# Kernel optimization log

Hardware: AMD Instinct MI355X
Metric: run time of the kernel (lower is better)

The kernel has to match this reference:

```python
import jax, jax.numpy as jnp
import numpy as np

LATENT = 64
HID = 64
IN_DIM = HID + 1  # 65
SLOPE = 0.2
EPS = 1e-8


def setup_inputs() -> dict:
    key = jax.random.key(0)
    ks = jax.random.split(key, 9)
    x = jax.random.normal(ks[0], (8192, LATENT, IN_DIM), dtype=jnp.float32)
    def init_w(k, shape, fan_in):
        return jax.random.uniform(k, shape, jnp.float32, -1.0, 1.0) / np.sqrt(fan_in)
    # Per-latent stacked MLP params: 3 LeakyReLU layers + final linear to scalar
    W0 = init_w(ks[1], (LATENT, HID, IN_DIM), IN_DIM)
    b0 = init_w(ks[2], (LATENT, HID), IN_DIM)
    W1 = init_w(ks[3], (LATENT, HID, HID), HID)
    b1 = init_w(ks[4], (LATENT, HID), HID)
    W2 = init_w(ks[5], (LATENT, HID, HID), HID)
    b2 = init_w(ks[6], (LATENT, HID), HID)
    W3 = init_w(ks[7], (LATENT, 1, HID), HID)
    b3 = init_w(ks[8], (LATENT, 1), HID)
    return {"x": x, "W0": W0, "b0": b0, "W1": W1, "b1": b1,
            "W2": W2, "b2": b2, "W3": W3, "b3": b3}


def _flow_single(w0, b0, w1, b1, w2, b2, w3, b3, xi):
    # xi: [B, IN_DIM] -> residual [B], d(out)/d(xi[:, -1]) [B]
    def f(z):
        h = jax.nn.leaky_relu(z @ w0.T + b0, SLOPE)
        h = jax.nn.leaky_relu(h @ w1.T + b1, SLOPE)
        h = jax.nn.leaky_relu(h @ w2.T + b2, SLOPE)
        return h @ w3.T + b3  # [B, 1]
    # only the last column of the Jacobian is used -> single batched JVP
    tan = jnp.zeros_like(xi).at[:, -1].set(1.0)
    out, dout = jax.jvp(f, (xi,), (tan,))
    return out[:, 0], dout[:, 0]


def reference(x, W0, b0, W1, b1, W2, b2, W3, b3):
    B = x.shape[0]
    # vmap over the latent axis (independent MLP per latent)
    residuals, dJ = jax.vmap(_flow_single,
                             in_axes=(0, 0, 0, 0, 0, 0, 0, 0, 1),
                             out_axes=(1, 1))(W0, b0, W1, b1, W2, b2, W3, b3, x)
    # residuals: [B, LATENT]; dJ: [B, LATENT]
    logabsdet = jnp.sum(jnp.log(jnp.abs(dJ) + EPS), axis=1)  # [B]
    return residuals.reshape(B, -1), logabsdet.reshape(B, -1)
```

## Files before the change

### kernel.cpp

```cpp
#include <hip/hip_runtime.h>
#include <hip/hip_bf16.h>
#include <cmath>

#define LATENTS 64
#define HID 64
#define IN_DIM 65
#define SLOPE 0.2f
#define FEPS 1e-8f
#define RPB 128
#define CHUNKS 8
#define WBYTES 53248
#define W65_BYTE (64 * WBYTES)

#define A_OF_SLOT(s) ((((((s) >> 2) & 1) * 2 + ((s) >> 5)) * 16) + ((((s) >> 3) & 3) * 4) + ((s) & 3))

typedef __attribute__((ext_vector_type(8))) short short8;
typedef __attribute__((ext_vector_type(4))) float f32x4;
typedef __attribute__((address_space(1))) const unsigned GASU;
typedef __attribute__((address_space(3))) unsigned LASU;

__device__ __forceinline__ unsigned asu(float f){ return __builtin_bit_cast(unsigned, f); }
__device__ __forceinline__ float    asf(unsigned u){ return __builtin_bit_cast(float, u); }
__device__ __forceinline__ unsigned bfu(float f){
    return (unsigned)__builtin_bit_cast(unsigned short, __float2bfloat16(f));
}

__device__ __forceinline__ void split8v(const float* f, short8& hi, short8& lo){
    unsigned hw[4], lw[4];
#pragma unroll
    for (int w = 0; w < 4; ++w){
        float a = f[2 * w], b = f[2 * w + 1];
        unsigned ua = bfu(a), ub = bfu(b);
        float la = a - asf(ua << 16), lb = b - asf(ub << 16);
        hw[w] = ua | (ub << 16);
        lw[w] = bfu(la) | (bfu(lb) << 16);
    }
    uint4 h4{hw[0], hw[1], hw[2], hw[3]}, l4{lw[0], lw[1], lw[2], lw[3]};
    hi = __builtin_bit_cast(short8, h4);
    lo = __builtin_bit_cast(short8, l4);
}

__device__ __forceinline__ void split8t(const float* f, short8& hi, short8& lo){
    unsigned hw[4], lw[4];
#pragma unroll
    for (int w = 0; w < 4; ++w){
        float a = f[2 * w], b = f[2 * w + 1];
        float la = a - asf(asu(a) & 0xFFFF0000u);
        float lb = b - asf(asu(b) & 0xFFFF0000u);
        hw[w] = __builtin_amdgcn_perm(asu(b), asu(a), 0x07060302u);
        lw[w] = __builtin_amdgcn_perm(asu(lb) + 0x8000u, asu(la) + 0x8000u, 0x07060302u);
    }
    uint4 h4{hw[0], hw[1], hw[2], hw[3]}, l4{lw[0], lw[1], lw[2], lw[3]};
    hi = __builtin_bit_cast(short8, h4);
    lo = __builtin_bit_cast(short8, l4);
}

__device__ __forceinline__ short8 pack8r(const float* f){
    unsigned w[4];
#pragma unroll
    for (int i = 0; i < 4; ++i)
        w[i] = __builtin_amdgcn_perm(asu(f[2 * i + 1]) + 0x8000u,
                                     asu(f[2 * i])     + 0x8000u, 0x07060302u);
    uint4 p{w[0], w[1], w[2], w[3]};
    return __builtin_bit_cast(short8, p);
}

__device__ __forceinline__ f32x4 mfma_(short8 a, short8 b, f32x4 c){
    return __builtin_amdgcn_mfma_f32_16x16x32_bf16(a, b, c, 0, 0, 0);
}

__global__ void lad_init_kernel(float* __restrict__ lad, int n){
    int i = blockIdx.x * blockDim.x + threadIdx.x;
    if (i < n) lad[i] = 0.0f;
}

__global__ __launch_bounds__(64)
void w_prep_kernel(const float* __restrict__ W0, const float* __restrict__ W1,
                   const float* __restrict__ W2, const float* __restrict__ W3,
                   char* __restrict__ ws)
{
    const int b = blockIdx.x;
    const int L = threadIdx.x;
    const int c  = L & 15;
    const int kb = (L >> 4) * 8;
    if (b < 192){
        const int l = b / 3, d = b - 3 * l;
        const float* Wd = (d == 0) ? W0 + (size_t)l * 64 * IN_DIM
                        : (d == 1) ? W1 + (size_t)l * 4096
                                   : W2 + (size_t)l * 4096;
        const int K = (d == 0) ? IN_DIM : 64;
#pragma unroll
        for (int ks = 0; ks < 2; ++ks)
#pragma unroll
            for (int ct = 0; ct < 4; ++ct){
                float wf[8];
#pragma unroll
                for (int j = 0; j < 8; ++j){
                    const int s = ks * 32 + kb + j;
                    const int a = (d == 0) ? s : A_OF_SLOT(s);
                    wf[j] = Wd[(size_t)(ct * 16 + c) * K + a];
                }
                short8 wh, wl;
                split8v(wf, wh, wl);
                char* base = ws + (size_t)l * WBYTES + d * 16384 + (ks * 4 + ct) * 1024 + L * 16;
                *(short8*)base            = wh;
                *(short8*)(base + 8192)   = wl;
            }
    } else {
        const int l = b - 192;
#pragma unroll
        for (int ks = 0; ks < 2; ++ks){
            float wf[8];
#pragma unroll
            for (int j = 0; j < 8; ++j)
                wf[j] = (c == 0) ? W3[l * 64 + A_OF_SLOT(ks * 32 + kb + j)] : 0.0f;
            short8 wh, wl;
            split8v(wf, wh, wl);
            char* base = ws + (size_t)l * WBYTES + 49152 + ks * 1024 + L * 16;
            *(short8*)base          = wh;
            *(short8*)(base + 2048) = wl;
        }
        ((float*)(ws + W65_BYTE))[l * 64 + L] =
            W0[(size_t)l * 64 * IN_DIM + L * IN_DIM + 64];
    }
}

__global__ __launch_bounds__(512, 4)
void flow_mfma_kernel(const float* __restrict__ x,
                      const float* __restrict__ b0, const float* __restrict__ b1,
                      const float* __restrict__ b2, const float* __restrict__ b3,
                      const char* __restrict__ ws,
                      float* __restrict__ out_res, float* __restrict__ out_lad)
{
    __shared__ __attribute__((aligned(16))) char wlds[WBYTES];

    const int l   = blockIdx.y;
    const int tid = threadIdx.x;
    const int L   = tid & 63;
    const int wv  = tid >> 6;
    const int u   = L >> 4;

    const char* gsrc = ws + (size_t)l * WBYTES;
#pragma unroll
    for (int i = 0; i < 7; ++i){
        const int base = i * 512 + wv * 64;
        if (base * 16 < WBYTES)
            __builtin_amdgcn_global_load_lds((GASU*)(gsrc + (base + L) * 16),
                                             (LASU*)(wlds + base * 16), 16, 0, 0);
    }
    __syncthreads();

    auto ldw = [&](int d, int ks, int ct, short8& wh, short8& wl){
        const char* p = wlds + d * 16384 + (ks * 4 + ct) * 1024 + (L << 4);
        wh = *(const short8*)p;
        wl = *(const short8*)(p + 8192);
    };

#pragma unroll 1
    for (int it = 0; it < CHUNKS; ++it){
        const int g0 = (blockIdx.x * CHUNKS + it) * RPB + wv * 16 + (L & 15);

        const float* xg0 = x + ((size_t)g0 * LATENTS + l) * IN_DIM;
        float xv[16];
#pragma unroll
        for (int j = 0; j < 8; ++j){
            xv[j]     = xg0[8 * u + j];
            xv[8 + j] = xg0[32 + 8 * u + j];
        }
        const float x65r = xg0[64];

        short8 bh[2], bl2[2], th2[2];
        split8t(&xv[0], bh[0], bl2[0]);
        split8t(&xv[8], bh[1], bl2[1]);

        f32x4 ha[4], ta[4];

        auto repack = [&](const float v[4][4], short8 (&hi)[2], short8 (&lo)[2]){
#pragma unroll
            for (int ks = 0; ks < 2; ++ks){
                float f8[8] = {v[ks][0], v[ks][1], v[ks][2], v[ks][3],
                               v[2 + ks][0], v[2 + ks][1], v[2 + ks][2], v[2 + ks][3]};
                split8t(f8, hi[ks], lo[ks]);
            }
        };
        auto repackt = [&](const float v[4][4], short8 (&hi)[2]){
#pragma unroll
            for (int ks = 0; ks < 2; ++ks){
                float f8[8] = {v[ks][0], v[ks][1], v[ks][2], v[ks][3],
                               v[2 + ks][0], v[2 + ks][1], v[2 + ks][2], v[2 + ks][3]};
                hi[ks] = pack8r(f8);
            }
        };

        {
#pragma unroll
            for (int ct = 0; ct < 4; ++ct)
                ha[ct] = __builtin_bit_cast(f32x4,
                            *(const float4*)(b0 + l * 64 + ct * 16 + u * 4));
#pragma unroll
            for (int ks = 0; ks < 2; ++ks){
#pragma unroll
                for (int ct = 0; ct < 4; ++ct){
                    short8 wh, wl;
                    ldw(0, ks, ct, wh, wl);
                    __builtin_amdgcn_s_setprio(1);
                    ha[ct] = mfma_(wh, bh[ks],  ha[ct]);
                    ha[ct] = mfma_(wh, bl2[ks], ha[ct]);
                    ha[ct] = mfma_(wl, bh[ks],  ha[ct]);
                    __builtin_amdgcn_s_setprio(0);
                }
            }
            const float* w65p = (const float*)(ws + W65_BYTE) + l * 64;
            float hv[4][4], tv[4][4];
#pragma unroll
            for (int ct = 0; ct < 4; ++ct){
                const float4 wv4 = *(const float4*)(w65p + ct * 16 + u * 4);
                const float wa[4] = {wv4.x, wv4.y, wv4.z, wv4.w};
#pragma unroll
                for (int i = 0; i < 4; ++i){
                    float z = fmaf(x65r, wa[i], ha[ct][i]);
                    float m = (z >= 0.0f) ? 1.0f : SLOPE;
                    hv[ct][i] = z * m;
                    tv[ct][i] = wa[i] * m;
                }
            }
            repack(hv, bh, bl2);
            repackt(tv, th2);
        }

        auto dense2 = [&](int d, const float* __restrict__ bl){
#pragma unroll
            for (int ct = 0; ct < 4; ++ct){
                ha[ct] = __builtin_bit_cast(f32x4,
                            *(const float4*)(bl + ct * 16 + u * 4));
                ta[ct] = (f32x4){0.f, 0.f, 0.f, 0.f};
            }
#pragma unroll
            for (int ks = 0; ks < 2; ++ks){
#pragma unroll
                for (int ct = 0; ct < 4; ++ct){
                    short8 wh, wl;
                    ldw(d, ks, ct, wh, wl);
                    __builtin_amdgcn_s_setprio(1);
                    ha[ct] = mfma_(wh, bh[ks],  ha[ct]);
                    ha[ct] = mfma_(wh, bl2[ks], ha[ct]);
                    ha[ct] = mfma_(wl, bh[ks],  ha[ct]);
                    ta[ct] = mfma_(wh, th2[ks], ta[ct]);
                    __builtin_amdgcn_s_setprio(0);
                }
            }
            float hv[4][4], tv[4][4];
#pragma unroll
            for (int ct = 0; ct < 4; ++ct)
#pragma unroll
                for (int i = 0; i < 4; ++i){
                    float z  = ha[ct][i];
                    float zt = ta[ct][i];
                    float m  = (z >= 0.0f) ? 1.0f : SLOPE;
                    hv[ct][i] = z * m;
                    tv[ct][i] = zt * m;
                }
            repack(hv, bh, bl2);
            repackt(tv, th2);
        };
        dense2(1, b1 + l * 64);
        dense2(2, b2 + l * 64);

        {
            f32x4 so = (f32x4){0.f, 0.f, 0.f, 0.f};
            f32x4 sd = (f32x4){0.f, 0.f, 0.f, 0.f};
#pragma unroll
            for (int ks = 0; ks < 2; ++ks){
                const char* p = wlds + 49152 + ks * 1024 + (L << 4);
                short8 wh = *(const short8*)p;
                short8 wl = *(const short8*)(p + 2048);
                __builtin_amdgcn_s_setprio(1);
                so = mfma_(wh, bh[ks],  so);
                so = mfma_(wh, bl2[ks], so);
                so = mfma_(wl, bh[ks],  so);
                sd = mfma_(wh, th2[ks], sd);
                __builtin_amdgcn_s_setprio(0);
            }
            if (u == 0){
                out_res[(size_t)g0 * LATENTS + l] = so[0] + b3[l];
                atomicAdd(&out_lad[g0], __logf(fabsf(sd[0]) + FEPS));
            }
        }
    }
}

extern "C" void kernel_launch(void* const* d_in, const int* in_sizes, int n_in,
                              void* d_out, int out_size, void* d_ws, size_t ws_size,
                              hipStream_t stream)
{
    const float* x  = (const float*)d_in[0];
    const float* W0 = (const float*)d_in[1];
    const float* b0 = (const float*)d_in[2];
    const float* W1 = (const float*)d_in[3];
    const float* b1 = (const float*)d_in[4];
    const float* W2 = (const float*)d_in[5];
    const float* b2 = (const float*)d_in[6];
    const float* W3 = (const float*)d_in[7];
    const float* b3 = (const float*)d_in[8];

    const int B = in_sizes[0] / (LATENTS * IN_DIM);
    float* out_res = (float*)d_out;
    float* out_lad = out_res + (size_t)B * LATENTS;
    char*  wsp     = (char*)d_ws;

    lad_init_kernel<<<dim3((B + 255) / 256), dim3(256), 0, stream>>>(out_lad, B);
    w_prep_kernel<<<dim3(256), dim3(64), 0, stream>>>(W0, W1, W2, W3, wsp);
    flow_mfma_kernel<<<dim3(B / (RPB * CHUNKS), LATENTS), dim3(512), 0, stream>>>(
        x, b0, b1, b2, b3, wsp, out_res, out_lad);
}
```

Before: 75.42 us.

## Software-pipeline x loads across chunks, halve chunks, add tangent low-part MFMA

Replaces the per-chunk loop with an explicitly unrolled four-chunk sequence that double-buffers x loads, prefetching the next chunk's inputs while the current chunk runs its MFMAs. The weight LDS fill is now overlapped with the first x loads. CHUNKS drops from 8 to 4, which doubles the grid. The high part in split8v now truncates instead of rounding, and the tangent path gains an extra MFMA with the low weight part for accuracy, which adds matrix work. Two xv buffers live at once, which raises register pressure.

```diff
diff --git a/kernel.cpp b/kernel.cpp
--- a/kernel.cpp
+++ b/kernel.cpp
@@ -8,7 +8,7 @@
 #define SLOPE 0.2f
 #define FEPS 1e-8f
 #define RPB 128
-#define CHUNKS 8
+#define CHUNKS 4
 #define WBYTES 53248
 #define W65_BYTE (64 * WBYTES)
 
@@ -30,9 +30,9 @@
 #pragma unroll
     for (int w = 0; w < 4; ++w){
         float a = f[2 * w], b = f[2 * w + 1];
-        unsigned ua = bfu(a), ub = bfu(b);
-        float la = a - asf(ua << 16), lb = b - asf(ub << 16);
-        hw[w] = ua | (ub << 16);
+        unsigned ha = asu(a) & 0xFFFF0000u, hb = asu(b) & 0xFFFF0000u;
+        float la = a - asf(ha), lb = b - asf(hb);
+        hw[w] = (ha >> 16) | hb;
         lw[w] = bfu(la) | (bfu(lb) << 16);
     }
     uint4 h4{hw[0], hw[1], hw[2], hw[3]}, l4{lw[0], lw[1], lw[2], lw[3]};
@@ -134,11 +134,12 @@
 {
     __shared__ __attribute__((aligned(16))) char wlds[WBYTES];
 
-    const int l   = blockIdx.y;
-    const int tid = threadIdx.x;
-    const int L   = tid & 63;
-    const int wv  = tid >> 6;
-    const int u   = L >> 4;
+    const int l     = blockIdx.y;
+    const int tid   = threadIdx.x;
+    const int L     = tid & 63;
+    const int wv    = tid >> 6;
+    const int u     = L >> 4;
+    const int rbase = blockIdx.x * (RPB * CHUNKS) + wv * 16 + (L & 15);
 
     const char* gsrc = ws + (size_t)l * WBYTES;
 #pragma unroll
@@ -148,49 +149,48 @@
             __builtin_amdgcn_global_load_lds((GASU*)(gsrc + (base + L) * 16),
                                              (LASU*)(wlds + base * 16), 16, 0, 0);
     }
-    __syncthreads();
+
+    auto loadx = [&](float (&xv)[16], float& x65, int c){
+        const float* xg = x + ((size_t)(rbase + c * RPB) * LATENTS + l) * IN_DIM;
+#pragma unroll
+        for (int j = 0; j < 8; ++j){
+            xv[j]     = xg[8 * u + j];
+            xv[8 + j] = xg[32 + 8 * u + j];
+        }
+        x65 = xg[64];
+    };
+
+    short8 bh[2], bl2[2], th2[2];
+    auto splitx = [&](const float (&xv)[16]){
+        split8t(&xv[0], bh[0], bl2[0]);
+        split8t(&xv[8], bh[1], bl2[1]);
+    };
 
     auto ldw = [&](int d, int ks, int ct, short8& wh, short8& wl){
         const char* p = wlds + d * 16384 + (ks * 4 + ct) * 1024 + (L << 4);
         wh = *(const short8*)p;
         wl = *(const short8*)(p + 8192);
     };
-
-#pragma unroll 1
-    for (int it = 0; it < CHUNKS; ++it){
-        const int g0 = (blockIdx.x * CHUNKS + it) * RPB + wv * 16 + (L & 15);
-
-        const float* xg0 = x + ((size_t)g0 * LATENTS + l) * IN_DIM;
-        float xv[16];
-#pragma unroll
-        for (int j = 0; j < 8; ++j){
-            xv[j]     = xg0[8 * u + j];
-            xv[8 + j] = xg0[32 + 8 * u + j];
-        }
-        const float x65r = xg0[64];
-
-        short8 bh[2], bl2[2], th2[2];
-        split8t(&xv[0], bh[0], bl2[0]);
-        split8t(&xv[8], bh[1], bl2[1]);
-
+    auto repack = [&](const float v[4][4]){
+#pragma unroll
+        for (int ks = 0; ks < 2; ++ks){
+            float f8[8] = {v[ks][0], v[ks][1], v[ks][2], v[ks][3],
+                           v[2 + ks][0], v[2 + ks][1], v[2 + ks][2], v[2 + ks][3]};
+            split8t(f8, bh[ks], bl2[ks]);
+        }
+    };
+    auto repackt = [&](const float v[4][4]){
+#pragma unroll
+        for (int ks = 0; ks < 2; ++ks){
+            float f8[8] = {v[ks][0], v[ks][1], v[ks][2], v[ks][3],
+                           v[2 + ks][0], v[2 + ks][1], v[2 + ks][2], v[2 + ks][3]};
+            th2[ks] = pack8r(f8);
+        }
+    };
+
+    auto run = [&](int c, float x65r){
+        const int g0 = rbase + c * RPB;
         f32x4 ha[4], ta[4];
-
-        auto repack = [&](const float v[4][4], short8 (&hi)[2], short8 (&lo)[2]){
-#pragma unroll
-            for (int ks = 0; ks < 2; ++ks){
-                float f8[8] = {v[ks][0], v[ks][1], v[ks][2], v[ks][3],
-                               v[2 + ks][0], v[2 + ks][1], v[2 + ks][2], v[2 + ks][3]};
-                split8t(f8, hi[ks], lo[ks]);
-            }
-        };
-        auto repackt = [&](const float v[4][4], short8 (&hi)[2]){
-#pragma unroll
-            for (int ks = 0; ks < 2; ++ks){
-                float f8[8] = {v[ks][0], v[ks][1], v[ks][2], v[ks][3],
-                               v[2 + ks][0], v[2 + ks][1], v[2 + ks][2], v[2 + ks][3]};
-                hi[ks] = pack8r(f8);
-            }
-        };
 
         {
 #pragma unroll
@@ -224,8 +224,8 @@
                     tv[ct][i] = wa[i] * m;
                 }
             }
-            repack(hv, bh, bl2);
-            repackt(tv, th2);
+            repack(hv);
+            repackt(tv);
         }
 
         auto dense2 = [&](int d, const float* __restrict__ bl){
@@ -246,6 +246,7 @@
                     ha[ct] = mfma_(wh, bl2[ks], ha[ct]);
                     ha[ct] = mfma_(wl, bh[ks],  ha[ct]);
                     ta[ct] = mfma_(wh, th2[ks], ta[ct]);
+                    ta[ct] = mfma_(wl, th2[ks], ta[ct]);
                     __builtin_amdgcn_s_setprio(0);
                 }
             }
@@ -260,8 +261,8 @@
                     hv[ct][i] = z * m;
                     tv[ct][i] = zt * m;
                 }
-            repack(hv, bh, bl2);
-            repackt(tv, th2);
+            repack(hv);
+            repackt(tv);
         };
         dense2(1, b1 + l * 64);
         dense2(2, b2 + l * 64);
@@ -279,6 +280,7 @@
                 so = mfma_(wh, bl2[ks], so);
                 so = mfma_(wl, bh[ks],  so);
                 sd = mfma_(wh, th2[ks], sd);
+                sd = mfma_(wl, th2[ks], sd);
                 __builtin_amdgcn_s_setprio(0);
             }
             if (u == 0){
@@ -286,7 +288,24 @@
                 atomicAdd(&out_lad[g0], __logf(fabsf(sd[0]) + FEPS));
             }
         }
-    }
+    };
+
+    float xvA[16], xvB[16];
+    float x650, x651, x652, x653;
+    loadx(xvA, x650, 0);
+    loadx(xvB, x651, 1);
+    __syncthreads();
+
+    splitx(xvA);
+    loadx(xvA, x652, 2);
+    run(0, x650);
+    splitx(xvB);
+    loadx(xvB, x653, 3);
+    run(1, x651);
+    splitx(xvA);
+    run(2, x652);
+    splitx(xvB);
+    run(3, x653);
 }
 
 extern "C" void kernel_launch(void* const* d_in, const int* in_sizes, int n_in,
```

Result: slower. 80.52 us (+6.8%).
